# Optimization experiments

Hardware: AMD Instinct MI355X
Metric: run time of the kernel (lower is better)

## Reference

```python
import jax, jax.numpy as jnp
import numpy as np


def _ln(x, g, b, eps=1e-5):
    m = x.mean(-1, keepdims=True)
    v = ((x - m) ** 2).mean(-1, keepdims=True)
    return (x - m) * jax.lax.rsqrt(v + eps) * g + b


def setup_inputs() -> dict:
    key = jax.random.key(0)
    ks = jax.random.split(key, 12)
    B, S, I, H, E, P, O, EM = 32, 512, 64, 512, 8, 96, 64, 512
    D = S * I
    r = lambda k, shape, s=0.02: jax.random.normal(k, shape, jnp.float32) * s
    z = lambda *shape: jnp.zeros(shape, jnp.float32)
    o = lambda *shape: jnp.ones(shape, jnp.float32)
    return dict(
        x=jax.random.normal(ks[0], (B, S, I), jnp.float32),
        gW1=r(ks[1], (D, EM)), gb1=z(EM), gln1_g=o(EM), gln1_b=z(EM),
        gW2=r(ks[2], (EM, EM)), gb2=z(EM), gln2_g=o(EM), gln2_b=z(EM),
        gW3=r(ks[3], (EM, 128)), gb3=z(128),
        protos=jax.random.normal(ks[4], (E, 128), jnp.float32) * 0.01,
        temp=jnp.ones((), jnp.float32),
        eW1=r(ks[5], (E, I, H)), eb1=z(E, H),
        eW2=r(ks[6], (E, H, H)), eb2=z(E, H),
        fW1=r(ks[7], (H, H)), fb1=z(H), fln_g=o(H), fln_b=z(H),
        fW2=r(ks[8], (H, H)), fb2=z(H),
        ln_g=o(H), ln_b=z(H),
        pW1=r(ks[9], (H, H // 2)), pb1=z(H // 2), pln_g=o(H // 2), pln_b=z(H // 2),
        pW2=r(ks[10], (H // 2, P * O)), pb2=z(P * O),
        on_g=o(O), on_b=z(O),
    )


def reference(x, gW1, gb1, gln1_g, gln1_b, gW2, gb2, gln2_g, gln2_b, gW3, gb3,
              protos, temp, eW1, eb1, eW2, eb2,
              fW1, fb1, fln_g, fln_b, fW2, fb2, ln_g, ln_b,
              pW1, pb1, pln_g, pln_b, pW2, pb2, on_g, on_b):
    B, S, I = x.shape
    O = on_g.shape[0]
    P = pW2.shape[1] // O
    # 1) flow latent mapping (identity fallback path of the original code)
    x_flat = x.reshape(B, S * I)
    z_latent = x_flat
    # 2) gating encoder -> 128-d embedding (dropout = identity in eval)
    h = jax.nn.relu(_ln(z_latent @ gW1 + gb1, gln1_g, gln1_b))
    h = jax.nn.relu(_ln(h @ gW2 + gb2, gln2_g, gln2_b))
    emb = h @ gW3 + gb3  # [B, 128]
    # 3) routing: euclidean cdist to prototypes, temperature-scaled softmax
    d2 = jnp.sum((emb[:, None, :] - protos[None, :, :]) ** 2, axis=-1)
    dist = jnp.sqrt(jnp.maximum(d2, 1e-12))  # [B, E]
    t = jnp.clip(temp, 0.1, 5.0)
    w = jax.nn.softmax(-dist / t, axis=-1)  # [B, E]
    # 4) experts: per-expert FFN on raw input, all experts batched
    he = jax.nn.relu(jnp.einsum('bsi,eih->besh', x, eW1) + eb1[None, :, None, :])
    eo = jnp.einsum('besh,eho->beso', he, eW2) + eb2[None, :, None, :]  # [B,E,S,H]
    # 5) routing-weighted combine + fusion + prediction head
    fused = jnp.einsum('besh,be->bsh', eo, w)
    f = jax.nn.relu(_ln(fused @ fW1 + fb1, fln_g, fln_b)) @ fW2 + fb2
    f = _ln(f, ln_g, ln_b)
    last = f[:, -1, :]  # [B, H]
    p = jax.nn.relu(_ln(last @ pW1 + pb1, pln_g, pln_b)) @ pW2 + pb2
    p = p.reshape(B, P, O)
    return _ln(p, on_g, on_b)
```

## Files before the change

kernel.cpp:

```cpp
#include <hip/hip_runtime.h>
#include <math.h>

#define DIMK 32768

__device__ __forceinline__ void fma4(float4& a, float s, const float4 w) {
  a.x += s * w.x; a.y += s * w.y; a.z += s * w.z; a.w += s * w.w;
}

__device__ __forceinline__ float fsel(const float4& v, int kk) {
  return kk == 0 ? v.x : kk == 1 ? v.y : kk == 2 ? v.z : v.w;
}

__device__ __forceinline__ void gld_lds16(const float* g, float* l) {
  __builtin_amdgcn_global_load_lds(
      (const __attribute__((address_space(1))) void*)g,
      (__attribute__((address_space(3))) void*)l, 16, 0, 0);
}

__device__ __forceinline__ float block_sum(float v, float* red, int n) {
  int t = threadIdx.x;
  red[t] = v;
  __syncthreads();
  for (int s = n >> 1; s > 0; s >>= 1) {
    if (t < s) red[t] += red[t + s];
    __syncthreads();
  }
  float r = red[0];
  __syncthreads();
  return r;
}

__global__ __launch_bounds__(256) void gemm1(const float* __restrict__ x,
                                             const float* __restrict__ gW1,
                                             float* __restrict__ part) {
  const int mt = blockIdx.x, ks = blockIdx.y;
  const int m0 = mt * 128, k0 = ks * 256;
  const int t = threadIdx.x;
  __shared__ float As[32 * 256];
  __shared__ float Ws[2][32 * 128];

  const float* Wp = gW1 + (size_t)k0 * 512 + m0;

#pragma unroll
  for (int j = 0; j < 8; ++j) {
    int i = t + j * 256;
    gld_lds16(x + (size_t)(i >> 6) * DIMK + k0 + (i & 63) * 4, &As[i * 4]);
  }
#pragma unroll
  for (int j = 0; j < 4; ++j) {
    int i = t + j * 256;
    gld_lds16(Wp + (size_t)(i >> 5) * 512 + (i & 31) * 4, &Ws[0][i * 4]);
  }

  const int mf4 = (t & 31) * 4;
  const int bg = t >> 5;
  float4 acc[4];
#pragma unroll
  for (int j = 0; j < 4; ++j) acc[j] = make_float4(0.f, 0.f, 0.f, 0.f);
  const float* a0 = &As[bg * 4 * 256];

  for (int s = 0; s < 8; ++s) {
    __syncthreads();
    if (s < 7) {
      const float* Wn = Wp + (size_t)(s + 1) * 32 * 512;
#pragma unroll
      for (int j = 0; j < 4; ++j) {
        int i = t + j * 256;
        gld_lds16(Wn + (size_t)(i >> 5) * 512 + (i & 31) * 4, &Ws[(s + 1) & 1][i * 4]);
      }
    }
    const float* Wc = Ws[s & 1];
    const int sc = s * 32;
#pragma unroll
    for (int kq = 0; kq < 8; ++kq) {
      float4 av0 = *(const float4*)(a0 + sc + kq * 4);
      float4 av1 = *(const float4*)(a0 + 256 + sc + kq * 4);
      float4 av2 = *(const float4*)(a0 + 512 + sc + kq * 4);
      float4 av3 = *(const float4*)(a0 + 768 + sc + kq * 4);
#pragma unroll
      for (int kk = 0; kk < 4; ++kk) {
        float4 wv = *(const float4*)&Wc[(kq * 4 + kk) * 128 + mf4];
        fma4(acc[0], fsel(av0, kk), wv);
        fma4(acc[1], fsel(av1, kk), wv);
        fma4(acc[2], fsel(av2, kk), wv);
        fma4(acc[3], fsel(av3, kk), wv);
      }
    }
  }

  float* op = part + ((size_t)ks * 32 + bg * 4) * 512 + m0 + mf4;
#pragma unroll
  for (int j = 0; j < 4; ++j) *(float4*)(op + (size_t)j * 512) = acc[j];
}

__global__ __launch_bounds__(512) void part_red(const float* __restrict__ part,
                                                float* __restrict__ pre) {
  const int b = blockIdx.x, c = blockIdx.y, t = threadIdx.x;
  float a = 0.f;
  const float* p = part + ((size_t)c * 16 * 32 + b) * 512 + t;
#pragma unroll
  for (int i = 0; i < 16; ++i) a += p[(size_t)i * 16384];
  pre[((size_t)c * 32 + b) * 512 + t] = a;
}

template <int KC>
__global__ __launch_bounds__(256) void gemm_tile(const float* __restrict__ A,
                                                 const float* __restrict__ W,
                                                 float* __restrict__ outp,
                                                 int M, int aRow,
                                                 size_t aStrideE, size_t wStrideE) {
  const int mt = blockIdx.x, kq = blockIdx.y, e = blockIdx.z, NE = gridDim.z;
  const int m0 = mt * 64, k0 = kq * KC;
  const int t = threadIdx.x;
  __shared__ float Ws[KC * 64];
  __shared__ float As[32 * (KC + 4)];
  const float* Wp = W + (size_t)e * wStrideE + (size_t)k0 * M + m0;
  for (int i = t; i < KC * 16; i += 256) {
    int r = i >> 4, q = i & 15;
    *(float4*)&Ws[r * 64 + q * 4] = *(const float4*)(Wp + (size_t)r * M + q * 4);
  }
  const float* Ap = A + (size_t)e * aStrideE + k0;
  for (int i = t; i < 32 * (KC / 4); i += 256) {
    int b = i / (KC / 4), q = i % (KC / 4);
    *(float4*)&As[b * (KC + 4) + q * 4] = *(const float4*)(Ap + (size_t)b * aRow + q * 4);
  }
  __syncthreads();
  const int mf = t & 15, bg = t >> 4;
  const int b0 = bg * 2;
  float4 acc0 = make_float4(0.f, 0.f, 0.f, 0.f), acc1 = acc0;
  const float* a0 = &As[b0 * (KC + 4)];
  const float* a1 = &As[(b0 + 1) * (KC + 4)];
#pragma unroll 8
  for (int k = 0; k < KC; ++k) {
    float4 wv = *(const float4*)&Ws[k * 64 + mf * 4];
    fma4(acc0, a0[k], wv);
    fma4(acc1, a1[k], wv);
  }
  float* op = outp + ((size_t)(kq * NE + e) * 32 + b0) * M + m0 + mf * 4;
  *(float4*)op = acc0;
  *(float4*)(op + M) = acc1;
}

__global__ void red_ln(const float* __restrict__ zp, const float* __restrict__ bias,
                       const float* __restrict__ g, const float* __restrict__ bt,
                       float* __restrict__ outp, int M, int nq, int relu) {
  const int b = blockIdx.x, t = threadIdx.x;
  __shared__ float red[512];
  float a = bias[t];
#pragma unroll 4
  for (int kq = 0; kq < nq; ++kq) a += zp[((size_t)kq * 32 + b) * M + t];
  float fM = 1.f / (float)M;
  float mean = block_sum(a, red, M) * fM;
  float d = a - mean;
  float var = block_sum(d * d, red, M) * fM;
  float v = d * rsqrtf(var + 1e-5f) * g[t] + bt[t];
  outp[b * M + t] = relu ? fmaxf(v, 0.f) : v;
}

__global__ __launch_bounds__(128) void gate_k(const float* __restrict__ zp2,
                                              const float* __restrict__ gb3,
                                              const float* __restrict__ protos,
                                              const float* __restrict__ temp,
                                              float* __restrict__ wgt) {
  __shared__ float red[128];
  __shared__ float d2s[8];
  const int b = blockIdx.x, t = threadIdx.x;
  float a = gb3[t];
#pragma unroll
  for (int kq = 0; kq < 8; ++kq) a += zp2[((size_t)kq * 32 + b) * 128 + t];
  for (int e = 0; e < 8; ++e) {
    float dd = a - protos[e * 128 + t];
    float s = block_sum(dd * dd, red, 128);
    if (t == 0) d2s[e] = s;
  }
  __syncthreads();
  if (t == 0) {
    float tt = fminf(fmaxf(temp[0], 0.1f), 5.0f);
    float lg[8], mx = -1e30f;
#pragma unroll
    for (int e = 0; e < 8; ++e) {
      float dist = sqrtf(fmaxf(d2s[e], 1e-12f));
      lg[e] = -dist / tt;
      mx = fmaxf(mx, lg[e]);
    }
    float se = 0.f;
#pragma unroll
    for (int e = 0; e < 8; ++e) { lg[e] = expf(lg[e] - mx); se += lg[e]; }
#pragma unroll
    for (int e = 0; e < 8; ++e) wgt[b * 8 + e] = lg[e] / se;
  }
}

__global__ __launch_bounds__(256) void he_k(const float* __restrict__ x,
                                            const float* __restrict__ eW1,
                                            const float* __restrict__ eb1,
                                            float* __restrict__ he_all) {
  const int e = blockIdx.x, hs = blockIdx.y;
  const int t = threadIdx.x;
  __shared__ float xs[32 * 64];
  __shared__ float Ws[64 * 256];
  for (int i = t; i < 512; i += 256) {
    int b = i >> 4, q = i & 15;
    *(float4*)&xs[b * 64 + q * 4] = *(const float4*)(x + (size_t)b * DIMK + 32704 + q * 4);
  }
  const float* w1 = eW1 + (size_t)e * 64 * 512 + hs * 256;
  for (int i = t; i < 64 * 64; i += 256) {
    int k = i >> 6, q = i & 63;
    *(float4*)&Ws[k * 256 + q * 4] = *(const float4*)(w1 + (size_t)k * 512 + q * 4);
  }
  __syncthreads();
  float acc[32];
#pragma unroll
  for (int b = 0; b < 32; ++b) acc[b] = 0.f;
#pragma unroll 4
  for (int k = 0; k < 64; ++k) {
    float wk = Ws[k * 256 + t];
#pragma unroll
    for (int b = 0; b < 32; ++b) acc[b] += xs[b * 64 + k] * wk;
  }
  float bb = eb1[e * 512 + hs * 256 + t];
  for (int b = 0; b < 32; ++b)
    he_all[((size_t)e * 32 + b) * 512 + hs * 256 + t] = fmaxf(acc[b] + bb, 0.f);
}

__global__ __launch_bounds__(128) void ffuse(const float* __restrict__ epart,
                                             const float* __restrict__ eb2,
                                             const float* __restrict__ wgt,
                                             float* __restrict__ fused) {
  const int b = blockIdx.x, t = blockIdx.y * 128 + threadIdx.x;
  __shared__ float wl[8];
  if (threadIdx.x < 8) wl[threadIdx.x] = wgt[b * 8 + threadIdx.x];
  __syncthreads();
  float a = 0.f;
#pragma unroll
  for (int e = 0; e < 8; ++e) {
    float s = eb2[e * 512 + t];
#pragma unroll
    for (int kq = 0; kq < 8; ++kq)
      s += epart[(((size_t)kq * 8 + e) * 32 + b) * 512 + t];
    a += wl[e] * s;
  }
  fused[b * 512 + t] = a;
}

__global__ __launch_bounds__(256) void fin_red(const float* __restrict__ fpart,
                                               const float* __restrict__ pb2,
                                               const float* __restrict__ ong,
                                               const float* __restrict__ onb,
                                               float* __restrict__ outp) {
  const int t = threadIdx.x;
  const int lane = t & 63, w = t >> 6;
  const int r = blockIdx.x * 4 + w;
  const int b = r / 96, pi = r % 96;
  const int m = pi * 64 + lane;
  float a = pb2[m];
#pragma unroll
  for (int kq = 0; kq < 4; ++kq) a += fpart[((size_t)kq * 32 + b) * 6144 + m];
  float s = a;
  s += __shfl_xor(s, 1); s += __shfl_xor(s, 2); s += __shfl_xor(s, 4);
  s += __shfl_xor(s, 8); s += __shfl_xor(s, 16); s += __shfl_xor(s, 32);
  float mean = s * (1.f / 64.f);
  float d = a - mean;
  float q = d * d;
  q += __shfl_xor(q, 1); q += __shfl_xor(q, 2); q += __shfl_xor(q, 4);
  q += __shfl_xor(q, 8); q += __shfl_xor(q, 16); q += __shfl_xor(q, 32);
  float rr = rsqrtf(q * (1.f / 64.f) + 1e-5f);
  outp[((size_t)b * 96 + pi) * 64 + lane] = d * rr * ong[lane] + onb[lane];
}

extern "C" void kernel_launch(void* const* d_in, const int* in_sizes, int n_in,
                              void* d_out, int out_size, void* d_ws, size_t ws_size,
                              hipStream_t stream) {
  (void)in_sizes; (void)n_in; (void)out_size; (void)ws_size;
  const float* x      = (const float*)d_in[0];
  const float* gW1    = (const float*)d_in[1];
  const float* gb1    = (const float*)d_in[2];
  const float* gln1_g = (const float*)d_in[3];
  const float* gln1_b = (const float*)d_in[4];
  const float* gW2    = (const float*)d_in[5];
  const float* gb2    = (const float*)d_in[6];
  const float* gln2_g = (const float*)d_in[7];
  const float* gln2_b = (const float*)d_in[8];
  const float* gW3    = (const float*)d_in[9];
  const float* gb3    = (const float*)d_in[10];
  const float* protos = (const float*)d_in[11];
  const float* temp   = (const float*)d_in[12];
  const float* eW1    = (const float*)d_in[13];
  const float* eb1    = (const float*)d_in[14];
  const float* eW2    = (const float*)d_in[15];
  const float* eb2    = (const float*)d_in[16];
  const float* fW1    = (const float*)d_in[17];
  const float* fb1    = (const float*)d_in[18];
  const float* fln_g  = (const float*)d_in[19];
  const float* fln_b  = (const float*)d_in[20];
  const float* fW2    = (const float*)d_in[21];
  const float* fb2    = (const float*)d_in[22];
  const float* ln_g   = (const float*)d_in[23];
  const float* ln_b   = (const float*)d_in[24];
  const float* pW1    = (const float*)d_in[25];
  const float* pb1    = (const float*)d_in[26];
  const float* pln_g  = (const float*)d_in[27];
  const float* pln_b  = (const float*)d_in[28];
  const float* pW2    = (const float*)d_in[29];
  const float* pb2    = (const float*)d_in[30];
  const float* on_g   = (const float*)d_in[31];
  const float* on_b   = (const float*)d_in[32];
  float* out = (float*)d_out;

  float* ws     = (float*)d_ws;
  float* part   = ws;
  float* epart  = ws;
  float* he_all = ws + 1048576;
  float* fpart  = ws;
  float* h1     = ws + 2097152;
  float* h2     = h1 + 16384;
  float* zp     = h2 + 16384;
  float* zp2    = zp + 262144;
  float* wgt    = zp2 + 65536;
  float* fused  = wgt + 256;
  float* f1     = fused + 16384;
  float* lastv  = f1 + 16384;
  float* pp     = lastv + 16384;

  gemm1<<<dim3(4, 128), 256, 0, stream>>>(x, gW1, part);
  part_red<<<dim3(32, 8), 512, 0, stream>>>(part, zp);
  red_ln<<<32, 512, 0, stream>>>(zp, gb1, gln1_g, gln1_b, h1, 512, 8, 1);
  gemm_tile<64><<<dim3(8, 8, 1), 256, 0, stream>>>(h1, gW2, zp, 512, 512, 0, 0);
  red_ln<<<32, 512, 0, stream>>>(zp, gb2, gln2_g, gln2_b, h2, 512, 8, 1);
  gemm_tile<64><<<dim3(2, 8, 1), 256, 0, stream>>>(h2, gW3, zp2, 128, 512, 0, 0);
  gate_k<<<32, 128, 0, stream>>>(zp2, gb3, protos, temp, wgt);

  he_k<<<dim3(8, 2), 256, 0, stream>>>(x, eW1, eb1, he_all);
  gemm_tile<64><<<dim3(8, 8, 8), 256, 0, stream>>>(he_all, eW2, epart, 512, 512,
                                                   (size_t)32 * 512, (size_t)512 * 512);
  ffuse<<<dim3(32, 4), 128, 0, stream>>>(epart, eb2, wgt, fused);

  gemm_tile<64><<<dim3(8, 8, 1), 256, 0, stream>>>(fused, fW1, zp, 512, 512, 0, 0);
  red_ln<<<32, 512, 0, stream>>>(zp, fb1, fln_g, fln_b, f1, 512, 8, 1);
  gemm_tile<64><<<dim3(8, 8, 1), 256, 0, stream>>>(f1, fW2, zp, 512, 512, 0, 0);
  red_ln<<<32, 512, 0, stream>>>(zp, fb2, ln_g, ln_b, lastv, 512, 8, 0);
  gemm_tile<64><<<dim3(4, 8, 1), 256, 0, stream>>>(lastv, pW1, zp, 256, 512, 0, 0);
  red_ln<<<32, 256, 0, stream>>>(zp, pb1, pln_g, pln_b, pp, 256, 8, 1);

  gemm_tile<64><<<dim3(96, 4, 1), 256, 0, stream>>>(pp, pW2, fpart, 6144, 256, 0, 0);
  fin_red<<<768, 256, 0, stream>>>(fpart, pb2, on_g, on_b, out);
}
```

Before: 276.8 us.

## Fuse small GEMMs with bias and LayerNorm into per-row kernels

Replaces the split-K gemm_tile plus red_ln pairs for the 512-wide MLP layers with a single per-batch-row kernel that computes the matvec, reduces partials in shared memory, and applies bias, LayerNorm and ReLU. The expert combine is folded into the first fusion layer, and the gate projection is merged with the prototype distance and softmax step. The expert and head GEMMs move to a larger K chunk so fewer partial sums are written. This cuts kernel launches and partial-sum round trips through global memory, but each fused layer runs on only 32 blocks, and every block streams the whole weight matrix.

```diff
diff --git a/kernel.cpp b/kernel.cpp
--- a/kernel.cpp
+++ b/kernel.cpp
@@ -101,6 +101,153 @@
 #pragma unroll
   for (int i = 0; i < 16; ++i) a += p[(size_t)i * 16384];
   pre[((size_t)c * 32 + b) * 512 + t] = a;
+}
+
+__global__ void red_ln(const float* __restrict__ zp, const float* __restrict__ bias,
+                       const float* __restrict__ g, const float* __restrict__ bt,
+                       float* __restrict__ outp, int M, int nq, int relu) {
+  const int b = blockIdx.x, t = threadIdx.x;
+  __shared__ float red[512];
+  float a = bias[t];
+#pragma unroll 4
+  for (int kq = 0; kq < nq; ++kq) a += zp[((size_t)kq * 32 + b) * M + t];
+  float fM = 1.f / (float)M;
+  float mean = block_sum(a, red, M) * fM;
+  float d = a - mean;
+  float var = block_sum(d * d, red, M) * fM;
+  float v = d * rsqrtf(var + 1e-5f) * g[t] + bt[t];
+  outp[b * M + t] = relu ? fmaxf(v, 0.f) : v;
+}
+
+template <int M, int RELU, int NFF>
+__global__ __launch_bounds__(512) void layer_ln(const float* __restrict__ A,
+                                                const float* __restrict__ W,
+                                                const float* __restrict__ bias,
+                                                const float* __restrict__ g,
+                                                const float* __restrict__ bt,
+                                                float* __restrict__ outp,
+                                                const float* __restrict__ wgt,
+                                                const float* __restrict__ eb2) {
+  constexpr int MG = M / 4;
+  constexpr int KG = 512 / MG;
+  constexpr int KPG = 512 / KG;
+  const int b = blockIdx.x, t = threadIdx.x;
+  __shared__ float Arow[512];
+  __shared__ float pacc[KG * M];
+  __shared__ float red[8];
+
+  if (NFF > 0) {
+    float s = 0.f;
+#pragma unroll
+    for (int e = 0; e < 8; ++e) {
+      float p = eb2[e * 512 + t];
+#pragma unroll
+      for (int kq = 0; kq < (NFF > 0 ? NFF : 1); ++kq)
+        p += A[(((size_t)kq * 8 + e) * 32 + b) * 512 + t];
+      s += wgt[b * 8 + e] * p;
+    }
+    Arow[t] = s;
+  } else {
+    Arow[t] = A[b * 512 + t];
+  }
+  __syncthreads();
+
+  const int m4 = (t % MG) * 4, kg = t / MG;
+  const float* Wp = W + (size_t)kg * KPG * M + m4;
+  float4 acc = make_float4(0.f, 0.f, 0.f, 0.f);
+  const float* ar = &Arow[kg * KPG];
+#pragma unroll 8
+  for (int k = 0; k < KPG; ++k) {
+    float4 wv = *(const float4*)(Wp + (size_t)k * M);
+    fma4(acc, ar[k], wv);
+  }
+  *(float4*)&pacc[kg * M + m4] = acc;
+  __syncthreads();
+
+  float a = 0.f;
+  const bool act = t < M;
+  if (act) {
+    a = bias[t];
+#pragma unroll
+    for (int k2 = 0; k2 < KG; ++k2) a += pacc[k2 * M + t];
+  }
+  const int lane = t & 63, wid = t >> 6;
+  float s = a;
+  s += __shfl_xor(s, 1); s += __shfl_xor(s, 2); s += __shfl_xor(s, 4);
+  s += __shfl_xor(s, 8); s += __shfl_xor(s, 16); s += __shfl_xor(s, 32);
+  if (lane == 0) red[wid] = s;
+  __syncthreads();
+  float tot = red[0] + red[1] + red[2] + red[3] + red[4] + red[5] + red[6] + red[7];
+  float mean = tot * (1.f / (float)M);
+  float d = act ? (a - mean) : 0.f;
+  __syncthreads();
+  float q = d * d;
+  q += __shfl_xor(q, 1); q += __shfl_xor(q, 2); q += __shfl_xor(q, 4);
+  q += __shfl_xor(q, 8); q += __shfl_xor(q, 16); q += __shfl_xor(q, 32);
+  if (lane == 0) red[wid] = q;
+  __syncthreads();
+  float tv = red[0] + red[1] + red[2] + red[3] + red[4] + red[5] + red[6] + red[7];
+  float var = tv * (1.f / (float)M);
+  if (act) {
+    float v = d * rsqrtf(var + 1e-5f) * g[t] + bt[t];
+    outp[b * M + t] = RELU ? fmaxf(v, 0.f) : v;
+  }
+}
+
+__global__ __launch_bounds__(512) void gate_fused(const float* __restrict__ h2,
+                                                  const float* __restrict__ gW3,
+                                                  const float* __restrict__ gb3,
+                                                  const float* __restrict__ protos,
+                                                  const float* __restrict__ temp,
+                                                  float* __restrict__ wgt) {
+  const int b = blockIdx.x, t = threadIdx.x;
+  __shared__ float Arow[512];
+  __shared__ float pacc[16 * 128];
+  __shared__ float emb[128];
+  __shared__ float d2s[8];
+  Arow[t] = h2[b * 512 + t];
+  __syncthreads();
+  const int m4 = (t & 31) * 4, kg = t >> 5;
+  const float* Wp = gW3 + (size_t)kg * 32 * 128 + m4;
+  float4 acc = make_float4(0.f, 0.f, 0.f, 0.f);
+  const float* ar = &Arow[kg * 32];
+#pragma unroll 8
+  for (int k = 0; k < 32; ++k) {
+    float4 wv = *(const float4*)(Wp + (size_t)k * 128);
+    fma4(acc, ar[k], wv);
+  }
+  *(float4*)&pacc[kg * 128 + m4] = acc;
+  __syncthreads();
+  if (t < 128) {
+    float a = gb3[t];
+#pragma unroll
+    for (int k2 = 0; k2 < 16; ++k2) a += pacc[k2 * 128 + t];
+    emb[t] = a;
+  }
+  __syncthreads();
+  const int lane = t & 63, wid = t >> 6;
+  float dd0 = emb[lane] - protos[wid * 128 + lane];
+  float dd1 = emb[lane + 64] - protos[wid * 128 + 64 + lane];
+  float q = dd0 * dd0 + dd1 * dd1;
+  q += __shfl_xor(q, 1); q += __shfl_xor(q, 2); q += __shfl_xor(q, 4);
+  q += __shfl_xor(q, 8); q += __shfl_xor(q, 16); q += __shfl_xor(q, 32);
+  if (lane == 0) d2s[wid] = q;
+  __syncthreads();
+  if (t == 0) {
+    float tt = fminf(fmaxf(temp[0], 0.1f), 5.0f);
+    float lg[8], mx = -1e30f;
+#pragma unroll
+    for (int e = 0; e < 8; ++e) {
+      float dist = sqrtf(fmaxf(d2s[e], 1e-12f));
+      lg[e] = -dist / tt;
+      mx = fmaxf(mx, lg[e]);
+    }
+    float se = 0.f;
+#pragma unroll
+    for (int e = 0; e < 8; ++e) { lg[e] = expf(lg[e] - mx); se += lg[e]; }
+#pragma unroll
+    for (int e = 0; e < 8; ++e) wgt[b * 8 + e] = lg[e] / se;
+  }
 }
 
 template <int KC>
@@ -141,56 +288,6 @@
   *(float4*)(op + M) = acc1;
 }
 
-__global__ void red_ln(const float* __restrict__ zp, const float* __restrict__ bias,
-                       const float* __restrict__ g, const float* __restrict__ bt,
-                       float* __restrict__ outp, int M, int nq, int relu) {
-  const int b = blockIdx.x, t = threadIdx.x;
-  __shared__ float red[512];
-  float a = bias[t];
-#pragma unroll 4
-  for (int kq = 0; kq < nq; ++kq) a += zp[((size_t)kq * 32 + b) * M + t];
-  float fM = 1.f / (float)M;
-  float mean = block_sum(a, red, M) * fM;
-  float d = a - mean;
-  float var = block_sum(d * d, red, M) * fM;
-  float v = d * rsqrtf(var + 1e-5f) * g[t] + bt[t];
-  outp[b * M + t] = relu ? fmaxf(v, 0.f) : v;
-}
-
-__global__ __launch_bounds__(128) void gate_k(const float* __restrict__ zp2,
-                                              const float* __restrict__ gb3,
-                                              const float* __restrict__ protos,
-                                              const float* __restrict__ temp,
-                                              float* __restrict__ wgt) {
-  __shared__ float red[128];
-  __shared__ float d2s[8];
-  const int b = blockIdx.x, t = threadIdx.x;
-  float a = gb3[t];
-#pragma unroll
-  for (int kq = 0; kq < 8; ++kq) a += zp2[((size_t)kq * 32 + b) * 128 + t];
-  for (int e = 0; e < 8; ++e) {
-    float dd = a - protos[e * 128 + t];
-    float s = block_sum(dd * dd, red, 128);
-    if (t == 0) d2s[e] = s;
-  }
-  __syncthreads();
-  if (t == 0) {
-    float tt = fminf(fmaxf(temp[0], 0.1f), 5.0f);
-    float lg[8], mx = -1e30f;
-#pragma unroll
-    for (int e = 0; e < 8; ++e) {
-      float dist = sqrtf(fmaxf(d2s[e], 1e-12f));
-      lg[e] = -dist / tt;
-      mx = fmaxf(mx, lg[e]);
-    }
-    float se = 0.f;
-#pragma unroll
-    for (int e = 0; e < 8; ++e) { lg[e] = expf(lg[e] - mx); se += lg[e]; }
-#pragma unroll
-    for (int e = 0; e < 8; ++e) wgt[b * 8 + e] = lg[e] / se;
-  }
-}
-
 __global__ __launch_bounds__(256) void he_k(const float* __restrict__ x,
                                             const float* __restrict__ eW1,
                                             const float* __restrict__ eb1,
@@ -223,26 +320,6 @@
     he_all[((size_t)e * 32 + b) * 512 + hs * 256 + t] = fmaxf(acc[b] + bb, 0.f);
 }
 
-__global__ __launch_bounds__(128) void ffuse(const float* __restrict__ epart,
-                                             const float* __restrict__ eb2,
-                                             const float* __restrict__ wgt,
-                                             float* __restrict__ fused) {
-  const int b = blockIdx.x, t = blockIdx.y * 128 + threadIdx.x;
-  __shared__ float wl[8];
-  if (threadIdx.x < 8) wl[threadIdx.x] = wgt[b * 8 + threadIdx.x];
-  __syncthreads();
-  float a = 0.f;
-#pragma unroll
-  for (int e = 0; e < 8; ++e) {
-    float s = eb2[e * 512 + t];
-#pragma unroll
-    for (int kq = 0; kq < 8; ++kq)
-      s += epart[(((size_t)kq * 8 + e) * 32 + b) * 512 + t];
-    a += wl[e] * s;
-  }
-  fused[b * 512 + t] = a;
-}
-
 __global__ __launch_bounds__(256) void fin_red(const float* __restrict__ fpart,
                                                const float* __restrict__ pb2,
                                                const float* __restrict__ ong,
@@ -255,7 +332,7 @@
   const int m = pi * 64 + lane;
   float a = pb2[m];
 #pragma unroll
-  for (int kq = 0; kq < 4; ++kq) a += fpart[((size_t)kq * 32 + b) * 6144 + m];
+  for (int kq = 0; kq < 2; ++kq) a += fpart[((size_t)kq * 32 + b) * 6144 + m];
   float s = a;
   s += __shfl_xor(s, 1); s += __shfl_xor(s, 2); s += __shfl_xor(s, 4);
   s += __shfl_xor(s, 8); s += __shfl_xor(s, 16); s += __shfl_xor(s, 32);
@@ -315,33 +392,29 @@
   float* h1     = ws + 2097152;
   float* h2     = h1 + 16384;
   float* zp     = h2 + 16384;
-  float* zp2    = zp + 262144;
-  float* wgt    = zp2 + 65536;
-  float* fused  = wgt + 256;
-  float* f1     = fused + 16384;
+  float* wgt    = zp + 262144;
+  float* f1     = wgt + 256;
   float* lastv  = f1 + 16384;
   float* pp     = lastv + 16384;
 
   gemm1<<<dim3(4, 128), 256, 0, stream>>>(x, gW1, part);
   part_red<<<dim3(32, 8), 512, 0, stream>>>(part, zp);
   red_ln<<<32, 512, 0, stream>>>(zp, gb1, gln1_g, gln1_b, h1, 512, 8, 1);
-  gemm_tile<64><<<dim3(8, 8, 1), 256, 0, stream>>>(h1, gW2, zp, 512, 512, 0, 0);
-  red_ln<<<32, 512, 0, stream>>>(zp, gb2, gln2_g, gln2_b, h2, 512, 8, 1);
-  gemm_tile<64><<<dim3(2, 8, 1), 256, 0, stream>>>(h2, gW3, zp2, 128, 512, 0, 0);
-  gate_k<<<32, 128, 0, stream>>>(zp2, gb3, protos, temp, wgt);
+  layer_ln<512, 1, 0><<<32, 512, 0, stream>>>(h1, gW2, gb2, gln2_g, gln2_b, h2,
+                                              nullptr, nullptr);
+  gate_fused<<<32, 512, 0, stream>>>(h2, gW3, gb3, protos, temp, wgt);
 
   he_k<<<dim3(8, 2), 256, 0, stream>>>(x, eW1, eb1, he_all);
-  gemm_tile<64><<<dim3(8, 8, 8), 256, 0, stream>>>(he_all, eW2, epart, 512, 512,
-                                                   (size_t)32 * 512, (size_t)512 * 512);
-  ffuse<<<dim3(32, 4), 128, 0, stream>>>(epart, eb2, wgt, fused);
-
-  gemm_tile<64><<<dim3(8, 8, 1), 256, 0, stream>>>(fused, fW1, zp, 512, 512, 0, 0);
-  red_ln<<<32, 512, 0, stream>>>(zp, fb1, fln_g, fln_b, f1, 512, 8, 1);
-  gemm_tile<64><<<dim3(8, 8, 1), 256, 0, stream>>>(f1, fW2, zp, 512, 512, 0, 0);
-  red_ln<<<32, 512, 0, stream>>>(zp, fb2, ln_g, ln_b, lastv, 512, 8, 0);
-  gemm_tile<64><<<dim3(4, 8, 1), 256, 0, stream>>>(lastv, pW1, zp, 256, 512, 0, 0);
-  red_ln<<<32, 256, 0, stream>>>(zp, pb1, pln_g, pln_b, pp, 256, 8, 1);
-
-  gemm_tile<64><<<dim3(96, 4, 1), 256, 0, stream>>>(pp, pW2, fpart, 6144, 256, 0, 0);
+  gemm_tile<128><<<dim3(8, 4, 8), 256, 0, stream>>>(he_all, eW2, epart, 512, 512,
+                                                    (size_t)32 * 512, (size_t)512 * 512);
+
+  layer_ln<512, 1, 4><<<32, 512, 0, stream>>>(epart, fW1, fb1, fln_g, fln_b, f1,
+                                              wgt, eb2);
+  layer_ln<512, 0, 0><<<32, 512, 0, stream>>>(f1, fW2, fb2, ln_g, ln_b, lastv,
+                                              nullptr, nullptr);
+  layer_ln<256, 1, 0><<<32, 512, 0, stream>>>(lastv, pW1, pb1, pln_g, pln_b, pp,
+                                              nullptr, nullptr);
+
+  gemm_tile<128><<<dim3(96, 2, 1), 256, 0, stream>>>(pp, pW2, fpart, 6144, 256, 0, 0);
   fin_red<<<768, 256, 0, stream>>>(fpart, pb2, on_g, on_b, out);
 }
```

New measurement: 304.3 us. 1.1x slower.
